# Performance work log

Hardware: AMD Instinct MI355X
Metric: run time of the kernel (lower is better)

## Reference

```python
import jax, jax.numpy as jnp
import numpy as np

N_HEAD, D_MODEL, D_HEAD = 16, 1024, 64
SEQ, BATCH = 1024, 8
SCALE = 1.0 / (D_HEAD ** 0.5)
LN_EPS = 1e-5


def setup_inputs() -> dict:
    key = jax.random.key(0)
    ks = jax.random.split(key, 16)
    dk = N_HEAD * D_HEAD  # == D_MODEL
    init_qkv = 1.0 / np.sqrt(D_MODEL)
    init_out = 1.0 / np.sqrt(dk)
    u = lambda k, shp, lo, hi: jax.random.uniform(k, shp, jnp.float32, lo, hi)
    inp = {
        'dec_inp': jax.random.normal(ks[0], (SEQ, BATCH, D_MODEL), jnp.float32),
        'attn_mask': jnp.triu(jnp.ones((SEQ, SEQ), dtype=bool), k=1),  # causal
        'query_mean': u(ks[1], (dk, D_MODEL), -init_qkv, init_qkv),
        'key_mean': u(ks[2], (dk, D_MODEL), -init_qkv, init_qkv),
        'value_mean': u(ks[3], (dk, D_MODEL), -init_qkv, init_qkv),
        'query_std': u(ks[4], (dk, D_MODEL), 2 * np.log(init_qkv), np.log(init_qkv)),
        'key_std': u(ks[5], (dk, D_MODEL), 2 * np.log(init_qkv), np.log(init_qkv)),
        'value_std': u(ks[6], (dk, D_MODEL), 2 * np.log(init_qkv), np.log(init_qkv)),
        'output_mean': u(ks[7], (D_MODEL, dk), -init_out, init_out),
        'output_std': u(ks[8], (D_MODEL, dk), 2 * np.log(init_out), np.log(init_out)),
        'ln_gamma': jnp.ones((D_MODEL,), jnp.float32),
        'ln_beta': jnp.zeros((D_MODEL,), jnp.float32),
        # per-forward reparameterization noise (training mode)
        'eps_q': jax.random.normal(ks[9], (dk, D_MODEL), jnp.float32),
        'eps_k': jax.random.normal(ks[10], (dk, D_MODEL), jnp.float32),
        'eps_v': jax.random.normal(ks[11], (dk, D_MODEL), jnp.float32),
        'eps_o': jax.random.normal(ks[12], (D_MODEL, dk), jnp.float32),
    }
    return inp


def _forward(dec_inp, query_mean, key_mean, value_mean, query_std, key_std,
             value_std, output_mean, output_std, ln_gamma, ln_beta,
             eps_q, eps_k, eps_v, eps_o, attn_mask):
    S, B, _ = dec_inp.shape
    # Bayesian weight sampling: w = mean + eps * exp(std)
    qw = query_mean + eps_q * jnp.exp(query_std)
    kw = key_mean + eps_k * jnp.exp(key_std)
    vw = value_mean + eps_v * jnp.exp(value_std)
    # NOTE: original code (bug kept for faithfulness) builds the output weight
    # from value_mean + output_diff, not output_mean.
    ow = value_mean + eps_o * jnp.exp(output_std)

    head_q = (dec_inp @ qw.T).reshape(S, B, N_HEAD, D_HEAD)
    head_k = (dec_inp @ kw.T).reshape(S, B, N_HEAD, D_HEAD)
    head_v = (dec_inp @ vw.T).reshape(S, B, N_HEAD, D_HEAD)

    score = jnp.einsum('ibnd,jbnd->ijbn', head_q, head_k) * SCALE
    score = jnp.where(attn_mask[:, :, None, None], -jnp.inf, score)
    prob = jax.nn.softmax(score, axis=1)  # softmax over j (key) axis
    attn_vec = jnp.einsum('ijbn,jbnd->ibnd', prob, head_v).reshape(S, B, N_HEAD * D_HEAD)

    attn_out = attn_vec @ ow.T
    x = dec_inp + attn_out
    mu = jnp.mean(x, axis=-1, keepdims=True)
    var = jnp.var(x, axis=-1, keepdims=True)
    output = (x - mu) * jax.lax.rsqrt(var + LN_EPS) * ln_gamma + ln_beta

    theta_mean = jnp.concatenate([query_mean, key_mean, value_mean, output_mean.T], -1)
    theta_std = jnp.concatenate([query_std, key_std, value_std, output_std.T], -1)
    kl = jnp.mean(theta_mean ** 2 - theta_std * 2.0 + jnp.exp(theta_std * 2.0)) / 2.0
    return output, kl


def reference(dec_inp, attn_mask, query_mean, key_mean, value_mean, query_std,
              key_std, value_std, output_mean, output_std, ln_gamma, ln_beta,
              eps_q, eps_k, eps_v, eps_o):
    return _forward(dec_inp, query_mean, key_mean, value_mean, query_std,
                    key_std, value_std, output_mean, output_std, ln_gamma,
                    ln_beta, eps_q, eps_k, eps_v, eps_o, attn_mask)
```

## Files before the change

### kernel.cpp

```cpp
#include <hip/hip_runtime.h>

typedef _Float16 f16x8 __attribute__((ext_vector_type(8)));
typedef _Float16 f16x4 __attribute__((ext_vector_type(4)));
typedef float    f32x4 __attribute__((ext_vector_type(4)));

static __device__ __forceinline__ f32x4 mfma16(f16x8 a, f16x8 b, f32x4 c) {
    return __builtin_amdgcn_mfma_f32_16x16x32_f16(a, b, c, 0, 0, 0);
}

static __device__ __forceinline__ void gload_lds16(const _Float16* g, _Float16* lds) {
    __builtin_amdgcn_global_load_lds(
        (const __attribute__((address_space(1))) unsigned int*)g,
        (__attribute__((address_space(3))) unsigned int*)lds, 16, 0, 0);
}

__global__ __launch_bounds__(256) void k_sample(
    const float* __restrict__ qm, const float* __restrict__ km, const float* __restrict__ vm,
    const float* __restrict__ qs, const float* __restrict__ ks, const float* __restrict__ vs,
    const float* __restrict__ om, const float* __restrict__ os,
    const float* __restrict__ eq, const float* __restrict__ ek,
    const float* __restrict__ ev, const float* __restrict__ eo,
    _Float16* __restrict__ wq, _Float16* __restrict__ wk,
    _Float16* __restrict__ wv, _Float16* __restrict__ wo,
    float* __restrict__ part)
{
    int i = blockIdx.x * 256 + threadIdx.x;
    float aqm = qm[i], akm = km[i], avm = vm[i];
    float aqs = qs[i], aks = ks[i], avs = vs[i];
    float aom = om[i], aos = os[i];
    wq[i] = (_Float16)(aqm + eq[i] * __expf(aqs));
    wk[i] = (_Float16)(akm + ek[i] * __expf(aks));
    wv[i] = (_Float16)(avm + ev[i] * __expf(avs));
    wo[i] = (_Float16)(avm + eo[i] * __expf(aos));
    float t = aqm*aqm - 2.f*aqs + __expf(2.f*aqs)
            + akm*akm - 2.f*aks + __expf(2.f*aks)
            + avm*avm - 2.f*avs + __expf(2.f*avs)
            + aom*aom - 2.f*aos + __expf(2.f*aos);
    #pragma unroll
    for (int m = 1; m < 64; m <<= 1) t += __shfl_xor(t, m, 64);
    __shared__ float red[4];
    int w = threadIdx.x >> 6, lane = threadIdx.x & 63;
    if (lane == 0) red[w] = t;
    __syncthreads();
    if (threadIdx.x == 0) part[blockIdx.x] = red[0] + red[1] + red[2] + red[3];
}

__global__ __launch_bounds__(256) void k_cvt(const float* __restrict__ in,
                                             _Float16* __restrict__ outh)
{
    int i = (blockIdx.x * 256 + threadIdx.x) * 4;
    float4 v = *(const float4*)&in[i];
    f16x4 hv;
    hv[0] = (_Float16)v.x; hv[1] = (_Float16)v.y;
    hv[2] = (_Float16)v.z; hv[3] = (_Float16)v.w;
    *(f16x4*)&outh[i] = hv;
}

__global__ __launch_bounds__(256) void k_gemm(
    const _Float16* __restrict__ A, const _Float16* __restrict__ B0,
    _Float16* __restrict__ C0, const float* __restrict__ resid,
    float* __restrict__ xout, int mode)
{
    __shared__ __align__(16) _Float16 As[128 * 64];
    __shared__ __align__(16) _Float16 Bs[128 * 64];
    const int K = 1024, N = 1024;
    const _Float16* Bp = B0 + (size_t)blockIdx.z * 1048576u;
    _Float16* Cp = C0 + (size_t)blockIdx.z * 8388608u;
    int tN = blockIdx.x * 128, tM = blockIdx.y * 128;
    int tid = threadIdx.x, w = tid >> 6, lane = tid & 63;
    int wm = w & 1, wn = w >> 1;
    int q = lane >> 4, r = lane & 15;
    f32x4 acc[4][4] = {};
    for (int kk = 0; kk < K; kk += 64) {
        __syncthreads();
        #pragma unroll
        for (int i = 0; i < 4; ++i) {
            int chunk = w * 4 + i;
            int row = chunk * 8 + (lane >> 3);
            int ko = (lane & 7) * 8;
            gload_lds16(A  + (size_t)(tM + row) * K + kk + ko, &As[chunk * 512]);
            gload_lds16(Bp + (size_t)(tN + row) * K + kk + ko, &Bs[chunk * 512]);
        }
        __syncthreads();
        #pragma unroll
        for (int kc = 0; kc < 2; ++kc) {
            f16x8 af[4], bf[4];
            #pragma unroll
            for (int m = 0; m < 4; ++m)
                af[m] = *(const f16x8*)&As[(wm*64 + m*16 + r)*64 + kc*32 + q*8];
            #pragma unroll
            for (int n = 0; n < 4; ++n)
                bf[n] = *(const f16x8*)&Bs[(wn*64 + n*16 + r)*64 + kc*32 + q*8];
            #pragma unroll
            for (int m = 0; m < 4; ++m)
                #pragma unroll
                for (int n = 0; n < 4; ++n)
                    acc[m][n] = mfma16(af[m], bf[n], acc[m][n]);
        }
    }
    float sc = (mode == 0 && blockIdx.z == 0) ? 0.125f : 1.0f;
    #pragma unroll
    for (int m = 0; m < 4; ++m)
      #pragma unroll
      for (int n = 0; n < 4; ++n)
        #pragma unroll
        for (int t = 0; t < 4; ++t) {
            int row = tM + wm*64 + m*16 + q*4 + t;
            int col = tN + wn*64 + n*16 + r;
            size_t o = (size_t)row * N + col;
            if (mode == 0) Cp[o] = (_Float16)(acc[m][n][t] * sc);
            else           xout[o] = resid[o] + acc[m][n][t];
        }
}

__global__ __launch_bounds__(256) void k_vtrans(const _Float16* __restrict__ V,
                                                _Float16* __restrict__ Vt)
{
    __shared__ __align__(16) _Float16 L[64 * 72];
    int c = blockIdx.x;
    int b = c >> 4, h = c & 15;
    int s0 = blockIdx.y * 64;
    int tid = threadIdx.x;
    #pragma unroll
    for (int rep = 0; rep < 2; ++rep) {
        int idx = rep * 256 + tid;
        int sl = idx >> 3, ch = idx & 7;
        f16x8 v = *(const f16x8*)&V[((size_t)(s0 + sl) * 8 + b) * 1024 + h * 64 + ch * 8];
        *(f16x8*)&L[sl * 72 + ch * 8] = v;
    }
    __syncthreads();
    #pragma unroll
    for (int rep = 0; rep < 2; ++rep) {
        int idx = rep * 256 + tid;
        int d = idx >> 3, c2 = idx & 7;
        f16x8 o;
        #pragma unroll
        for (int e = 0; e < 8; ++e) o[e] = L[(c2 * 8 + e) * 72 + d];
        *(f16x8*)&Vt[((size_t)c * 64 + d) * 1024 + s0 + c2 * 8] = o;
    }
}

__global__ __launch_bounds__(256, 4) void k_attn(
    const _Float16* __restrict__ Qb, const _Float16* __restrict__ Kb,
    const _Float16* __restrict__ Vtg, _Float16* __restrict__ AVo)
{
    __shared__ __align__(16) _Float16 Ks[64 * 64];
    __shared__ __align__(16) _Float16 Vs[64 * 64];
    __shared__ __align__(16) _Float16 Ps[4 * 32 * 72];
    const int bh = blockIdx.x;
    const int b = bh & 7, h = bh >> 3;
    const int cbh = b * 16 + h;
    const int qt = blockIdx.y;
    const int tid = threadIdx.x, w = tid >> 6, lane = tid & 63;
    const int q = lane >> 4, r = lane & 15;
    const int i0 = qt * 128 + w * 32;

    f16x8 qf[2][2];
    #pragma unroll
    for (int it = 0; it < 2; ++it)
      #pragma unroll
      for (int kc = 0; kc < 2; ++kc)
        qf[it][kc] = *(const f16x8*)&Qb[((size_t)(i0 + it*16 + r)*8 + b)*1024 + h*64 + kc*32 + q*8];

    f32x4 ot[4][2] = {};
    float mrun[2] = {-1e30f, -1e30f}, lrun[2] = {0.f, 0.f};
    _Float16* Pw = &Ps[w * 2304];

    auto tile = [&](int kt, bool MASK) __attribute__((always_inline)) {
        __syncthreads();
        #pragma unroll
        for (int ii = 0; ii < 2; ++ii) {
            int chunk = w * 2 + ii;
            int row = chunk * 8 + (lane >> 3);
            int co = (lane & 7) * 8;
            gload_lds16(Kb  + ((size_t)(kt*64 + row)*8 + b)*1024 + h*64 + co, &Ks[chunk*512]);
            gload_lds16(Vtg + ((size_t)(cbh*64 + row))*1024 + kt*64 + co,     &Vs[chunk*512]);
        }
        __syncthreads();

        f32x4 st[4][2] = {};
        #pragma unroll
        for (int kc = 0; kc < 2; ++kc) {
            f16x8 kf[4];
            #pragma unroll
            for (int jt = 0; jt < 4; ++jt)
                kf[jt] = *(const f16x8*)&Ks[(jt*16 + r)*64 + kc*32 + q*8];
            #pragma unroll
            for (int jt = 0; jt < 4; ++jt)
              #pragma unroll
              for (int it = 0; it < 2; ++it)
                st[jt][it] = mfma16(kf[jt], qf[it][kc], st[jt][it]);
        }

        #pragma unroll
        for (int it = 0; it < 2; ++it) {
            if (MASK) {
                int il = i0 + it*16 + r;
                #pragma unroll
                for (int jt = 0; jt < 4; ++jt)
                  #pragma unroll
                  for (int t = 0; t < 4; ++t)
                    if (kt*64 + jt*16 + q*4 + t > il) st[jt][it][t] = -1e30f;
            }
            float mx = -1e30f;
            #pragma unroll
            for (int jt = 0; jt < 4; ++jt) {
                f32x4 s4 = st[jt][it];
                mx = fmaxf(mx, fmaxf(fmaxf(s4[0], s4[1]), fmaxf(s4[2], s4[3])));
            }
            mx = fmaxf(mx, __shfl_xor(mx, 16, 64));
            mx = fmaxf(mx, __shfl_xor(mx, 32, 64));
            float mnew = fmaxf(mrun[it], mx);
            float al = __expf(mrun[it] - mnew);
            mrun[it] = mnew;
            float ps = 0.f;
            #pragma unroll
            for (int jt = 0; jt < 4; ++jt) {
                f16x4 hv;
                #pragma unroll
                for (int t = 0; t < 4; ++t) {
                    float e = __expf(st[jt][it][t] - mnew);
                    ps += e;
                    hv[t] = (_Float16)e;
                }
                *(f16x4*)&Pw[(it*16 + r)*72 + jt*16 + q*4] = hv;
            }
            ps += __shfl_xor(ps, 16, 64);
            ps += __shfl_xor(ps, 32, 64);
            lrun[it] = lrun[it] * al + ps;
            #pragma unroll
            for (int dtb = 0; dtb < 4; ++dtb) ot[dtb][it] *= al;
        }

        #pragma unroll
        for (int kc = 0; kc < 2; ++kc) {
            f16x8 vf[4], pf[2];
            #pragma unroll
            for (int dtb = 0; dtb < 4; ++dtb)
                vf[dtb] = *(const f16x8*)&Vs[(dtb*16 + r)*64 + kc*32 + q*8];
            #pragma unroll
            for (int it = 0; it < 2; ++it)
                pf[it] = *(const f16x8*)&Pw[(it*16 + r)*72 + kc*32 + q*8];
            #pragma unroll
            for (int dtb = 0; dtb < 4; ++dtb)
              #pragma unroll
              for (int it = 0; it < 2; ++it)
                ot[dtb][it] = mfma16(vf[dtb], pf[it], ot[dtb][it]);
        }
    };

    for (int kt = 0; kt < 2*qt; ++kt) tile(kt, false);
    tile(2*qt,     true);
    tile(2*qt + 1, true);

    #pragma unroll
    for (int it = 0; it < 2; ++it) {
        float inv = 1.f / lrun[it];
        int s = i0 + it*16 + r;
        #pragma unroll
        for (int dtb = 0; dtb < 4; ++dtb) {
            f16x4 hv;
            #pragma unroll
            for (int t = 0; t < 4; ++t) hv[t] = (_Float16)(ot[dtb][it][t] * inv);
            *(f16x4*)&AVo[((size_t)s*8 + b)*1024 + h*64 + dtb*16 + q*4] = hv;
        }
    }
}

__global__ __launch_bounds__(256) void k_ln(float* __restrict__ x,
    const float* __restrict__ g, const float* __restrict__ bta)
{
    int row = blockIdx.x;
    float* xr = x + (size_t)row * 1024;
    int t4 = threadIdx.x * 4;
    float4 v = *(const float4*)&xr[t4];
    float s  = v.x + v.y + v.z + v.w;
    float s2 = v.x*v.x + v.y*v.y + v.z*v.z + v.w*v.w;
    #pragma unroll
    for (int m = 1; m < 64; m <<= 1) { s += __shfl_xor(s, m, 64); s2 += __shfl_xor(s2, m, 64); }
    __shared__ float rs[4], rs2[4];
    int w = threadIdx.x >> 6, lane = threadIdx.x & 63;
    if (lane == 0) { rs[w] = s; rs2[w] = s2; }
    __syncthreads();
    s  = rs[0] + rs[1] + rs[2] + rs[3];
    s2 = rs2[0] + rs2[1] + rs2[2] + rs2[3];
    float mu = s * (1.f / 1024.f);
    float var = s2 * (1.f / 1024.f) - mu * mu;
    float rstd = rsqrtf(var + 1e-5f);
    float4 gv = *(const float4*)&g[t4];
    float4 bv = *(const float4*)&bta[t4];
    float4 ov;
    ov.x = (v.x - mu) * rstd * gv.x + bv.x;
    ov.y = (v.y - mu) * rstd * gv.y + bv.y;
    ov.z = (v.z - mu) * rstd * gv.z + bv.z;
    ov.w = (v.w - mu) * rstd * gv.w + bv.w;
    *(float4*)&xr[t4] = ov;
}

__global__ __launch_bounds__(256) void k_klfin(const float* __restrict__ part,
                                               float* __restrict__ out)
{
    float s = 0.f;
    for (int i = threadIdx.x; i < 4096; i += 256) s += part[i];
    #pragma unroll
    for (int m = 1; m < 64; m <<= 1) s += __shfl_xor(s, m, 64);
    __shared__ float red[4];
    int w = threadIdx.x >> 6, lane = threadIdx.x & 63;
    if (lane == 0) red[w] = s;
    __syncthreads();
    if (threadIdx.x == 0)
        out[8388608] = (red[0] + red[1] + red[2] + red[3]) * (0.5f / 4194304.f);
}

extern "C" void kernel_launch(void* const* d_in, const int* in_sizes, int n_in,
                              void* d_out, int out_size, void* d_ws, size_t ws_size,
                              hipStream_t stream)
{
    (void)in_sizes; (void)n_in; (void)out_size; (void)ws_size;
    const float* dec   = (const float*)d_in[0];
    const float* qm    = (const float*)d_in[2];
    const float* km    = (const float*)d_in[3];
    const float* vm    = (const float*)d_in[4];
    const float* qs    = (const float*)d_in[5];
    const float* ks    = (const float*)d_in[6];
    const float* vs    = (const float*)d_in[7];
    const float* om    = (const float*)d_in[8];
    const float* os    = (const float*)d_in[9];
    const float* gamma = (const float*)d_in[10];
    const float* beta  = (const float*)d_in[11];
    const float* eq    = (const float*)d_in[12];
    const float* ek    = (const float*)d_in[13];
    const float* ev    = (const float*)d_in[14];
    const float* eo    = (const float*)d_in[15];

    char* ws = (char*)d_ws;
    _Float16* WQ   = (_Float16*)ws;
    float*    PART = (float*)(ws + (8ull  << 20));
    _Float16* XH   = (_Float16*)(ws + (9ull  << 20));
    _Float16* Qh   = (_Float16*)(ws + (25ull << 20));
    _Float16* Kh   = Qh + 8388608;
    _Float16* Vh   = Qh + 16777216;
    _Float16* Vtg  = XH;
    _Float16* AV   = Vh;
    float*    out  = (float*)d_out;

    k_sample<<<dim3(4096), dim3(256), 0, stream>>>(
        qm, km, vm, qs, ks, vs, om, os, eq, ek, ev, eo,
        WQ, WQ + 1048576, WQ + 2097152, WQ + 3145728, PART);
    k_cvt<<<dim3(8192), dim3(256), 0, stream>>>(dec, XH);
    k_gemm<<<dim3(8, 64, 3), dim3(256), 0, stream>>>(XH, WQ, Qh, dec, out, 0);
    k_vtrans<<<dim3(128, 16), dim3(256), 0, stream>>>(Vh, Vtg);
    k_attn<<<dim3(128, 8), dim3(256), 0, stream>>>(Qh, Kh, Vtg, AV);
    k_gemm<<<dim3(8, 64, 1), dim3(256), 0, stream>>>(AV, WQ + 3145728, Qh, dec, out, 1);
    k_ln<<<dim3(8192), dim3(256), 0, stream>>>(out, gamma, beta);
    k_klfin<<<dim3(1), dim3(256), 0, stream>>>(PART, out);
}
```

Baseline: 366.7 us.

## XOR-swizzle LDS tiles in GEMM/attention and merge small kernels into neighbors

Adds an XOR swizzle to the global-to-LDS load column mapping and the matching fragment reads in the GEMM and attention kernels. The goal is to remove LDS bank conflicts on the 16-byte row-strided fragment reads. It also folds the fp16 input conversion into the weight-sampling kernel and the KL final reduction into the layernorm kernel, which cuts two launches. The swizzle adds some index arithmetic, and the merged kernels carry a branch on the block index.

```diff
diff --git a/kernel.cpp b/kernel.cpp
--- a/kernel.cpp
+++ b/kernel.cpp
@@ -14,7 +14,7 @@
         (__attribute__((address_space(3))) unsigned int*)lds, 16, 0, 0);
 }
 
-__global__ __launch_bounds__(256) void k_sample(
+__global__ __launch_bounds__(256) void k_prep(
     const float* __restrict__ qm, const float* __restrict__ km, const float* __restrict__ vm,
     const float* __restrict__ qs, const float* __restrict__ ks, const float* __restrict__ vs,
     const float* __restrict__ om, const float* __restrict__ os,
@@ -22,8 +22,18 @@
     const float* __restrict__ ev, const float* __restrict__ eo,
     _Float16* __restrict__ wq, _Float16* __restrict__ wk,
     _Float16* __restrict__ wv, _Float16* __restrict__ wo,
-    float* __restrict__ part)
-{
+    float* __restrict__ part,
+    const float* __restrict__ dec, _Float16* __restrict__ xh)
+{
+    if (blockIdx.x >= 4096) {
+        int i = ((blockIdx.x - 4096) * 256 + threadIdx.x) * 4;
+        float4 v = *(const float4*)&dec[i];
+        f16x4 hv;
+        hv[0] = (_Float16)v.x; hv[1] = (_Float16)v.y;
+        hv[2] = (_Float16)v.z; hv[3] = (_Float16)v.w;
+        *(f16x4*)&xh[i] = hv;
+        return;
+    }
     int i = blockIdx.x * 256 + threadIdx.x;
     float aqm = qm[i], akm = km[i], avm = vm[i];
     float aqs = qs[i], aks = ks[i], avs = vs[i];
@@ -45,17 +55,6 @@
     if (threadIdx.x == 0) part[blockIdx.x] = red[0] + red[1] + red[2] + red[3];
 }
 
-__global__ __launch_bounds__(256) void k_cvt(const float* __restrict__ in,
-                                             _Float16* __restrict__ outh)
-{
-    int i = (blockIdx.x * 256 + threadIdx.x) * 4;
-    float4 v = *(const float4*)&in[i];
-    f16x4 hv;
-    hv[0] = (_Float16)v.x; hv[1] = (_Float16)v.y;
-    hv[2] = (_Float16)v.z; hv[3] = (_Float16)v.w;
-    *(f16x4*)&outh[i] = hv;
-}
-
 __global__ __launch_bounds__(256) void k_gemm(
     const _Float16* __restrict__ A, const _Float16* __restrict__ B0,
     _Float16* __restrict__ C0, const float* __restrict__ resid,
@@ -70,27 +69,34 @@
     int tid = threadIdx.x, w = tid >> 6, lane = tid & 63;
     int wm = w & 1, wn = w >> 1;
     int q = lane >> 4, r = lane & 15;
+    int csrc = ((lane & 7) ^ (lane >> 3)) * 8;
+    int srow = lane >> 3;
     f32x4 acc[4][4] = {};
     for (int kk = 0; kk < K; kk += 64) {
         __syncthreads();
         #pragma unroll
         for (int i = 0; i < 4; ++i) {
             int chunk = w * 4 + i;
-            int row = chunk * 8 + (lane >> 3);
-            int ko = (lane & 7) * 8;
-            gload_lds16(A  + (size_t)(tM + row) * K + kk + ko, &As[chunk * 512]);
-            gload_lds16(Bp + (size_t)(tN + row) * K + kk + ko, &Bs[chunk * 512]);
+            int row = chunk * 8 + srow;
+            gload_lds16(A  + (size_t)(tM + row) * K + kk + csrc, &As[chunk * 512]);
+            gload_lds16(Bp + (size_t)(tN + row) * K + kk + csrc, &Bs[chunk * 512]);
         }
         __syncthreads();
         #pragma unroll
         for (int kc = 0; kc < 2; ++kc) {
             f16x8 af[4], bf[4];
             #pragma unroll
-            for (int m = 0; m < 4; ++m)
-                af[m] = *(const f16x8*)&As[(wm*64 + m*16 + r)*64 + kc*32 + q*8];
-            #pragma unroll
-            for (int n = 0; n < 4; ++n)
-                bf[n] = *(const f16x8*)&Bs[(wn*64 + n*16 + r)*64 + kc*32 + q*8];
+            for (int m = 0; m < 4; ++m) {
+                int row = wm*64 + m*16 + r;
+                int pos = ((kc*4 + q) ^ (r & 7)) * 8;
+                af[m] = *(const f16x8*)&As[row*64 + pos];
+            }
+            #pragma unroll
+            for (int n = 0; n < 4; ++n) {
+                int row = wn*64 + n*16 + r;
+                int pos = ((kc*4 + q) ^ (r & 7)) * 8;
+                bf[n] = *(const f16x8*)&Bs[row*64 + pos];
+            }
             #pragma unroll
             for (int m = 0; m < 4; ++m)
                 #pragma unroll
@@ -154,6 +160,8 @@
     const int tid = threadIdx.x, w = tid >> 6, lane = tid & 63;
     const int q = lane >> 4, r = lane & 15;
     const int i0 = qt * 128 + w * 32;
+    const int csrc = ((lane & 7) ^ (lane >> 3)) * 8;
+    const int srow = lane >> 3;
 
     f16x8 qf[2][2];
     #pragma unroll
@@ -171,10 +179,9 @@
         #pragma unroll
         for (int ii = 0; ii < 2; ++ii) {
             int chunk = w * 2 + ii;
-            int row = chunk * 8 + (lane >> 3);
-            int co = (lane & 7) * 8;
-            gload_lds16(Kb  + ((size_t)(kt*64 + row)*8 + b)*1024 + h*64 + co, &Ks[chunk*512]);
-            gload_lds16(Vtg + ((size_t)(cbh*64 + row))*1024 + kt*64 + co,     &Vs[chunk*512]);
+            int row = chunk * 8 + srow;
+            gload_lds16(Kb  + ((size_t)(kt*64 + row)*8 + b)*1024 + h*64 + csrc, &Ks[chunk*512]);
+            gload_lds16(Vtg + ((size_t)(cbh*64 + row))*1024 + kt*64 + csrc,     &Vs[chunk*512]);
         }
         __syncthreads();
 
@@ -183,8 +190,10 @@
         for (int kc = 0; kc < 2; ++kc) {
             f16x8 kf[4];
             #pragma unroll
-            for (int jt = 0; jt < 4; ++jt)
-                kf[jt] = *(const f16x8*)&Ks[(jt*16 + r)*64 + kc*32 + q*8];
+            for (int jt = 0; jt < 4; ++jt) {
+                int pos = ((kc*4 + q) ^ (r & 7)) * 8;
+                kf[jt] = *(const f16x8*)&Ks[(jt*16 + r)*64 + pos];
+            }
             #pragma unroll
             for (int jt = 0; jt < 4; ++jt)
               #pragma unroll
@@ -236,8 +245,10 @@
         for (int kc = 0; kc < 2; ++kc) {
             f16x8 vf[4], pf[2];
             #pragma unroll
-            for (int dtb = 0; dtb < 4; ++dtb)
-                vf[dtb] = *(const f16x8*)&Vs[(dtb*16 + r)*64 + kc*32 + q*8];
+            for (int dtb = 0; dtb < 4; ++dtb) {
+                int pos = ((kc*4 + q) ^ (r & 7)) * 8;
+                vf[dtb] = *(const f16x8*)&Vs[(dtb*16 + r)*64 + pos];
+            }
             #pragma unroll
             for (int it = 0; it < 2; ++it)
                 pf[it] = *(const f16x8*)&Pw[(it*16 + r)*72 + kc*32 + q*8];
@@ -268,8 +279,22 @@
 }
 
 __global__ __launch_bounds__(256) void k_ln(float* __restrict__ x,
-    const float* __restrict__ g, const float* __restrict__ bta)
-{
+    const float* __restrict__ g, const float* __restrict__ bta,
+    const float* __restrict__ part)
+{
+    __shared__ float rs[4], rs2[4];
+    int w = threadIdx.x >> 6, lane = threadIdx.x & 63;
+    if (blockIdx.x == 8192) {
+        float s = 0.f;
+        for (int i = threadIdx.x; i < 4096; i += 256) s += part[i];
+        #pragma unroll
+        for (int m = 1; m < 64; m <<= 1) s += __shfl_xor(s, m, 64);
+        if (lane == 0) rs[w] = s;
+        __syncthreads();
+        if (threadIdx.x == 0)
+            x[8388608] = (rs[0] + rs[1] + rs[2] + rs[3]) * (0.5f / 4194304.f);
+        return;
+    }
     int row = blockIdx.x;
     float* xr = x + (size_t)row * 1024;
     int t4 = threadIdx.x * 4;
@@ -278,8 +303,6 @@
     float s2 = v.x*v.x + v.y*v.y + v.z*v.z + v.w*v.w;
     #pragma unroll
     for (int m = 1; m < 64; m <<= 1) { s += __shfl_xor(s, m, 64); s2 += __shfl_xor(s2, m, 64); }
-    __shared__ float rs[4], rs2[4];
-    int w = threadIdx.x >> 6, lane = threadIdx.x & 63;
     if (lane == 0) { rs[w] = s; rs2[w] = s2; }
     __syncthreads();
     s  = rs[0] + rs[1] + rs[2] + rs[3];
@@ -295,21 +318,6 @@
     ov.z = (v.z - mu) * rstd * gv.z + bv.z;
     ov.w = (v.w - mu) * rstd * gv.w + bv.w;
     *(float4*)&xr[t4] = ov;
-}
-
-__global__ __launch_bounds__(256) void k_klfin(const float* __restrict__ part,
-                                               float* __restrict__ out)
-{
-    float s = 0.f;
-    for (int i = threadIdx.x; i < 4096; i += 256) s += part[i];
-    #pragma unroll
-    for (int m = 1; m < 64; m <<= 1) s += __shfl_xor(s, m, 64);
-    __shared__ float red[4];
-    int w = threadIdx.x >> 6, lane = threadIdx.x & 63;
-    if (lane == 0) red[w] = s;
-    __syncthreads();
-    if (threadIdx.x == 0)
-        out[8388608] = (red[0] + red[1] + red[2] + red[3]) * (0.5f / 4194304.f);
 }
 
 extern "C" void kernel_launch(void* const* d_in, const int* in_sizes, int n_in,
@@ -344,14 +352,12 @@
     _Float16* AV   = Vh;
     float*    out  = (float*)d_out;
 
-    k_sample<<<dim3(4096), dim3(256), 0, stream>>>(
+    k_prep<<<dim3(12288), dim3(256), 0, stream>>>(
         qm, km, vm, qs, ks, vs, om, os, eq, ek, ev, eo,
-        WQ, WQ + 1048576, WQ + 2097152, WQ + 3145728, PART);
-    k_cvt<<<dim3(8192), dim3(256), 0, stream>>>(dec, XH);
+        WQ, WQ + 1048576, WQ + 2097152, WQ + 3145728, PART, dec, XH);
     k_gemm<<<dim3(8, 64, 3), dim3(256), 0, stream>>>(XH, WQ, Qh, dec, out, 0);
     k_vtrans<<<dim3(128, 16), dim3(256), 0, stream>>>(Vh, Vtg);
     k_attn<<<dim3(128, 8), dim3(256), 0, stream>>>(Qh, Kh, Vtg, AV);
     k_gemm<<<dim3(8, 64, 1), dim3(256), 0, stream>>>(AV, WQ + 3145728, Qh, dec, out, 1);
-    k_ln<<<dim3(8192), dim3(256), 0, stream>>>(out, gamma, beta);
-    k_klfin<<<dim3(1), dim3(256), 0, stream>>>(PART, out);
-}
+    k_ln<<<dim3(8193), dim3(256), 0, stream>>>(out, gamma, beta, PART);
+}
```

Result: faster. 355.4 us (-3.1%).
